# Kernel tuning notes

Hardware: AMD Instinct MI355X
Metric: run time of the kernel (lower is better)

The kernel has to match this reference:

```python
import jax, jax.numpy as jnp
import numpy as np

N_HEAD = 16
ROPE_BASE = 10000.0


def _rope(x, cos, sin):
    # x: [B,H,T,D]; cos/sin: [T,D/2] broadcast over B,H
    half = x.shape[-1] // 2
    x1, x2 = x[..., :half], x[..., half:]
    return jnp.concatenate([x1 * cos - x2 * sin, x1 * sin + x2 * cos], axis=-1)


def setup_inputs() -> dict:
    key = jax.random.key(0)
    k1, k2, k3 = jax.random.split(key, 3)
    C = 2048
    x = jax.random.normal(k1, (4, 2048, C), dtype=jnp.float32)
    w_qkv = jax.random.normal(k2, (C, 3 * C), dtype=jnp.float32) * 0.02
    w_proj = jax.random.normal(k3, (C, C), dtype=jnp.float32) * 0.02
    return {"x": x, "w_qkv": w_qkv, "w_proj": w_proj}


def reference(x, w_qkv, w_proj):
    B, T, C = x.shape
    H = N_HEAD
    D = C // H
    half = D // 2

    qkv = x @ w_qkv  # [B,T,3C]
    q, k, v = jnp.split(qkv, 3, axis=-1)
    # [B,T,C] -> [B,H,T,D]
    q = q.reshape(B, T, H, D).transpose(0, 2, 1, 3)
    k = k.reshape(B, T, H, D).transpose(0, 2, 1, 3)
    v = v.reshape(B, T, H, D).transpose(0, 2, 1, 3)

    # RoPE cache (start_pos = 0, no kv_cache / prefill path)
    inv_freq = 1.0 / (ROPE_BASE ** (jnp.arange(half, dtype=jnp.float32) / half))
    pos = jnp.arange(T, dtype=jnp.float32)
    freqs = pos[:, None] * inv_freq[None, :]  # [T, half]
    cos, sin = jnp.cos(freqs), jnp.sin(freqs)

    q = _rope(q, cos, sin)
    k = _rope(k, cos, sin)

    # scaled dot-product attention with explicit causal mask
    att = jnp.einsum("bhqd,bhkd->bhqk", q, k) / jnp.sqrt(jnp.asarray(D, x.dtype))
    causal = jnp.arange(T)[:, None] >= jnp.arange(T)[None, :]  # [T,T] bool
    att = jnp.where(causal, att, jnp.asarray(-jnp.inf, att.dtype))
    att = jax.nn.softmax(att, axis=-1)
    # dropout = identity (eval mode)
    out = jnp.einsum("bhqk,bhkd->bhqd", att, v)
    out = out.transpose(0, 2, 1, 3).reshape(B, T, C)
    out = out @ w_proj
    return out, k, v  # (output, new kv-cache)
```

## Files before the change

kernel.cpp:

```cpp
#include <hip/hip_runtime.h>
#include <math.h>

#define CDIM 2048
#define TDIM 2048
#define BDIM 4
#define HDIM 16
#define DDIM 128
#define M1   (BDIM * TDIM)
#define N1   (3 * CDIM)
#define KK   CDIM

typedef unsigned short u16;
typedef __bf16 bf16x8 __attribute__((ext_vector_type(8)));
typedef float f32x4 __attribute__((ext_vector_type(4)));

__device__ __forceinline__ u16 f2b(float f) {
  union { float f; unsigned u; } x; x.f = f;
  unsigned r = x.u + 0x7fffu + ((x.u >> 16) & 1u);
  return (u16)(r >> 16);
}

__device__ __forceinline__ void gload_lds16(const void* g, void* l) {
  __builtin_amdgcn_global_load_lds(
      (__attribute__((address_space(1))) void*)g,
      (__attribute__((address_space(3))) void*)l, 16, 0, 0);
}

__global__ void convert_x(const float* __restrict__ x, u16* __restrict__ xb, int n4) {
  int i = blockIdx.x * blockDim.x + threadIdx.x;
  if (i < n4) {
    float4 v = ((const float4*)x)[i];
    unsigned long long o = (unsigned long long)f2b(v.x)
                         | ((unsigned long long)f2b(v.y) << 16)
                         | ((unsigned long long)f2b(v.z) << 32)
                         | ((unsigned long long)f2b(v.w) << 48);
    ((unsigned long long*)xb)[i] = o;
  }
}

__global__ void transpose_w(const float* __restrict__ w, u16* __restrict__ wt, int K, int N) {
  __shared__ float tile[32][33];
  const int n0 = blockIdx.x * 32, k0 = blockIdx.y * 32;
  const int tx = threadIdx.x & 31, ty = threadIdx.x >> 5;
  for (int r = ty; r < 32; r += 8)
    tile[r][tx] = w[(k0 + r) * N + n0 + tx];
  __syncthreads();
  for (int r = ty; r < 32; r += 8)
    wt[(n0 + r) * K + k0 + tx] = f2b(tile[tx][r]);
}

__global__ void rope_tab(float* __restrict__ cosT, float* __restrict__ sinT) {
  int i = blockIdx.x * blockDim.x + threadIdx.x;
  int t = i >> 6, d = i & 63;
  double inv = pow(10000.0, -(double)d / 64.0);
  double a = (double)t * inv;
  cosT[i] = (float)cos(a);
  sinT[i] = (float)sin(a);
}

__global__ void transpose_v(const float* __restrict__ v, u16* __restrict__ vt) {
  __shared__ float tile[32][33];
  const int bh = blockIdx.z;
  const int t0 = blockIdx.x * 32, d0 = blockIdx.y * 32;
  const int tx = threadIdx.x & 31, ty = threadIdx.x >> 5;
  const float* src = v + (bh * TDIM + t0) * DDIM + d0;
  for (int r = ty; r < 32; r += 8)
    tile[r][tx] = src[r * DDIM + tx];
  __syncthreads();
  u16* dst = vt + (bh * DDIM + d0) * TDIM + t0;
  for (int r = ty; r < 32; r += 8)
    dst[r * TDIM + tx] = f2b(tile[tx][r]);
}

__global__ __launch_bounds__(256, 2) void gemm_qkv(
    const u16* __restrict__ A,
    const u16* __restrict__ Bt,
    const float* __restrict__ cosT, const float* __restrict__ sinT,
    u16* __restrict__ qb, u16* __restrict__ kb,
    float* __restrict__ kout, float* __restrict__ vout)
{
  __shared__ __attribute__((aligned(16))) union {
    struct { u16 A[128 * 32]; u16 B[128 * 32]; } st;
    float c[64 * 128];
  } sm;
  const int tid = threadIdx.x;
  const int wave = tid >> 6, lane = tid & 63;
  const int quad = lane >> 4, c16 = lane & 15;
  const int m0 = blockIdx.y * 128, n0 = blockIdx.x * 128;
  const int wm = (wave >> 1) * 64, wn = (wave & 1) * 64;

  f32x4 acc[4][4];
  f32x4 zero = {0.f, 0.f, 0.f, 0.f};
#pragma unroll
  for (int i = 0; i < 4; ++i)
#pragma unroll
    for (int j = 0; j < 4; ++j) acc[i][j] = zero;

  const u16* Ab = A + m0 * KK;
  const u16* Bb = Bt + n0 * KK;
  const int rowA = wave * 16 + (lane >> 2);
  const int kof = (lane & 3) * 8;

  for (int k0 = 0; k0 < KK; k0 += 32) {
#pragma unroll
    for (int r = 0; r < 2; ++r) {
      gload_lds16(Ab + (r * 64 + rowA) * KK + k0 + kof, &sm.st.A[(r * 64 + wave * 16) * 32]);
      gload_lds16(Bb + (r * 64 + rowA) * KK + k0 + kof, &sm.st.B[(r * 64 + wave * 16) * 32]);
    }
    __syncthreads();
    bf16x8 af[4], bf_[4];
#pragma unroll
    for (int i = 0; i < 4; ++i) af[i]  = *(const bf16x8*)&sm.st.A[(wm + i * 16 + c16) * 32 + quad * 8];
#pragma unroll
    for (int j = 0; j < 4; ++j) bf_[j] = *(const bf16x8*)&sm.st.B[(wn + j * 16 + c16) * 32 + quad * 8];
#pragma unroll
    for (int i = 0; i < 4; ++i)
#pragma unroll
      for (int j = 0; j < 4; ++j)
        acc[i][j] = __builtin_amdgcn_mfma_f32_16x16x32_bf16(af[i], bf_[j], acc[i][j], 0, 0, 0);
    __syncthreads();
  }

  const int mat = n0 >> 11;
  const int h = (n0 & 2047) >> 7;
  const float qscale = 0.088388347648318447f;
  for (int pass = 0; pass < 2; ++pass) {
    __syncthreads();
    if ((wave >> 1) == pass) {
#pragma unroll
      for (int i = 0; i < 4; ++i)
#pragma unroll
        for (int j = 0; j < 4; ++j)
#pragma unroll
          for (int r = 0; r < 4; ++r)
            sm.c[(i * 16 + quad * 4 + r) * 128 + wn + j * 16 + c16] = acc[i][j][r];
    }
    __syncthreads();
    for (int it = 0; it < 16; ++it) {
      int p = it * 256 + tid;
      int lr = p >> 6;
      int d = p & 63;
      float x1 = sm.c[lr * 128 + d];
      float x2 = sm.c[lr * 128 + 64 + d];
      int mg = m0 + pass * 64 + lr;
      int b = mg >> 11, t = mg & 2047;
      int idx = ((b * HDIM + h) * TDIM + t) * DDIM + d;
      if (mat == 2) {
        vout[idx] = x1; vout[idx + 64] = x2;
      } else {
        float cs = cosT[t * 64 + d], sn = sinT[t * 64 + d];
        float o1 = x1 * cs - x2 * sn;
        float o2 = x1 * sn + x2 * cs;
        if (mat == 0) {
          qb[idx] = f2b(o1 * qscale); qb[idx + 64] = f2b(o2 * qscale);
        } else {
          kout[idx] = o1; kout[idx + 64] = o2;
          kb[idx] = f2b(o1); kb[idx + 64] = f2b(o2);
        }
      }
    }
  }
}

__global__ __launch_bounds__(256, 2) void attn(
    const u16* __restrict__ qb, const u16* __restrict__ kb,
    const u16* __restrict__ vt, u16* __restrict__ att)
{
  __shared__ __attribute__((aligned(16))) u16 sh[24576];
  u16* const ksm = sh;
  u16* const vsm = sh + 8192;
  u16* const psm = sh + 16384;

  const int tid = threadIdx.x, wave = tid >> 6, lane = tid & 63;
  const int quad = lane >> 4, c16 = lane & 15;
  const int bx = blockIdx.x;
  const int bh = blockIdx.y;

  for (int hv = 0; hv < 2; ++hv) {
    const int qt = hv ? (7 - bx) : (bx + 8);
    const int q0 = qt * 128;

    {
      const u16* qg = qb + (bh * TDIM + q0) * DDIM;
      const int rowl = wave * 4 + (lane >> 4);
      const int ch = lane & 15;
#pragma unroll
      for (int r = 0; r < 8; ++r) {
        int row = r * 16 + rowl;
        gload_lds16(qg + row * DDIM + (ch ^ (row & 15)) * 8,
                    &sh[(r * 16 + wave * 4) * 128]);
      }
    }
    __syncthreads();
    bf16x8 qf[2][4];
#pragma unroll
    for (int g = 0; g < 2; ++g)
#pragma unroll
      for (int kp = 0; kp < 4; ++kp)
        qf[g][kp] = *(const bf16x8*)&sh[(g * 64 + wave * 16 + c16) * 128 +
                                        (((kp * 4 + quad) ^ c16) * 8)];
    __syncthreads();

    f32x4 o[2][8];
    f32x4 zero = {0.f, 0.f, 0.f, 0.f};
#pragma unroll
    for (int g = 0; g < 2; ++g)
#pragma unroll
      for (int jd = 0; jd < 8; ++jd) o[g][jd] = zero;
    float mrow[2][4], lrow[2][4];
#pragma unroll
    for (int g = 0; g < 2; ++g)
#pragma unroll
      for (int r = 0; r < 4; ++r) { mrow[g][r] = -INFINITY; lrow[g][r] = 0.f; }

    const int nchunk = 2 * qt + 2;
    for (int kc = 0; kc < nchunk; ++kc) {
      const int kc0 = kc * 64;
      {
        const u16* kg = kb + (bh * TDIM + kc0) * DDIM;
        const int rowl = wave * 4 + (lane >> 4);
        const int ch = lane & 15;
#pragma unroll
        for (int r = 0; r < 4; ++r) {
          int row = r * 16 + rowl;
          gload_lds16(kg + row * DDIM + (ch ^ (row & 15)) * 8,
                      &ksm[(r * 16 + wave * 4) * 128]);
        }
        const u16* vg = vt + bh * (DDIM * TDIM) + kc0;
        const int rowv = wave * 8 + (lane >> 3);
        const int chv = lane & 7;
#pragma unroll
        for (int r = 0; r < 4; ++r) {
          int row = r * 32 + rowv;
          gload_lds16(vg + row * TDIM + (chv ^ (row & 7)) * 8,
                      &vsm[(r * 32 + wave * 8) * 64]);
        }
      }
      __syncthreads();

      f32x4 st[2][4];
#pragma unroll
      for (int g = 0; g < 2; ++g)
#pragma unroll
        for (int j = 0; j < 4; ++j) st[g][j] = zero;
#pragma unroll
      for (int kp = 0; kp < 4; ++kp) {
#pragma unroll
        for (int j = 0; j < 4; ++j) {
          bf16x8 bk = *(const bf16x8*)&ksm[(j * 16 + c16) * 128 +
                                           (((kp * 4 + quad) ^ c16) * 8)];
          st[0][j] = __builtin_amdgcn_mfma_f32_16x16x32_bf16(qf[0][kp], bk, st[0][j], 0, 0, 0);
          st[1][j] = __builtin_amdgcn_mfma_f32_16x16x32_bf16(qf[1][kp], bk, st[1][j], 0, 0, 0);
        }
      }

      u16* const pw = psm + wave * 2048;
      float al2[2][4];
#pragma unroll
      for (int g = 0; g < 2; ++g) {
        const bool dg = (kc >= 2 * qt + g);
        const int qrow_base = q0 + g * 64 + wave * 16 + quad * 4;
#pragma unroll
        for (int r = 0; r < 4; ++r) {
          float mx = -INFINITY;
#pragma unroll
          for (int j = 0; j < 4; ++j) {
            float sv = st[g][j][r];
            if (dg && (kc0 + j * 16 + c16 > qrow_base + r)) sv = -INFINITY;
            st[g][j][r] = sv;
            mx = fmaxf(mx, sv);
          }
          mx = fmaxf(mx, __shfl_xor(mx, 1, 64));
          mx = fmaxf(mx, __shfl_xor(mx, 2, 64));
          mx = fmaxf(mx, __shfl_xor(mx, 4, 64));
          mx = fmaxf(mx, __shfl_xor(mx, 8, 64));
          float mnew = fmaxf(mrow[g][r], mx);
          float al = __expf(mrow[g][r] - mnew);
          mrow[g][r] = mnew;
          al2[g][r] = al;
          float sum = 0.f;
          const int row16 = quad * 4 + r;
#pragma unroll
          for (int j = 0; j < 4; ++j) {
            float p = __expf(st[g][j][r] - mnew);
            sum += p;
            int chunk = (j * 2 + (c16 >> 3)) ^ (row16 & 7);
            pw[g * 1024 + row16 * 64 + chunk * 8 + (c16 & 7)] = f2b(p);
          }
          sum += __shfl_xor(sum, 1, 64);
          sum += __shfl_xor(sum, 2, 64);
          sum += __shfl_xor(sum, 4, 64);
          sum += __shfl_xor(sum, 8, 64);
          lrow[g][r] = lrow[g][r] * al + sum;
        }
#pragma unroll
        for (int jd = 0; jd < 8; ++jd)
#pragma unroll
          for (int r = 0; r < 4; ++r)
            o[g][jd][r] *= al2[g][r];
      }

      asm volatile("s_waitcnt lgkmcnt(0)" ::: "memory");

#pragma unroll
      for (int s = 0; s < 2; ++s) {
        const int chp = ((s * 4 + quad) ^ (c16 & 7)) * 8;
        bf16x8 ap0 = *(const bf16x8*)&pw[c16 * 64 + chp];
        bf16x8 ap1 = *(const bf16x8*)&pw[1024 + c16 * 64 + chp];
#pragma unroll
        for (int jd = 0; jd < 8; ++jd) {
          bf16x8 bv = *(const bf16x8*)&vsm[(jd * 16 + c16) * 64 + chp];
          o[0][jd] = __builtin_amdgcn_mfma_f32_16x16x32_bf16(ap0, bv, o[0][jd], 0, 0, 0);
          o[1][jd] = __builtin_amdgcn_mfma_f32_16x16x32_bf16(ap1, bv, o[1][jd], 0, 0, 0);
        }
      }
      __syncthreads();
    }

    const int b = bh >> 4, h = bh & 15;
#pragma unroll
    for (int g = 0; g < 2; ++g) {
      float ri[4];
#pragma unroll
      for (int r = 0; r < 4; ++r) ri[r] = 1.f / lrow[g][r];
#pragma unroll
      for (int jd = 0; jd < 8; ++jd)
#pragma unroll
        for (int r = 0; r < 4; ++r) {
          int t = q0 + g * 64 + wave * 16 + quad * 4 + r;
          att[(b * TDIM + t) * CDIM + h * DDIM + jd * 16 + c16] = f2b(o[g][jd][r] * ri[r]);
        }
    }
  }
}

__global__ __launch_bounds__(256, 2) void gemm_proj(
    const u16* __restrict__ A,
    const u16* __restrict__ Bt,
    float* __restrict__ out)
{
  __shared__ __attribute__((aligned(16))) struct { u16 A[128 * 32]; u16 B[128 * 32]; } sm;
  const int tid = threadIdx.x;
  const int wave = tid >> 6, lane = tid & 63;
  const int quad = lane >> 4, c16 = lane & 15;
  const int m0 = blockIdx.y * 128, n0 = blockIdx.x * 128;
  const int wm = (wave >> 1) * 64, wn = (wave & 1) * 64;

  f32x4 acc[4][4];
  f32x4 zero = {0.f, 0.f, 0.f, 0.f};
#pragma unroll
  for (int i = 0; i < 4; ++i)
#pragma unroll
    for (int j = 0; j < 4; ++j) acc[i][j] = zero;

  const u16* Ab = A + m0 * KK;
  const u16* Bb = Bt + n0 * KK;
  const int rowA = wave * 16 + (lane >> 2);
  const int kof = (lane & 3) * 8;

  for (int k0 = 0; k0 < KK; k0 += 32) {
#pragma unroll
    for (int r = 0; r < 2; ++r) {
      gload_lds16(Ab + (r * 64 + rowA) * KK + k0 + kof, &sm.A[(r * 64 + wave * 16) * 32]);
      gload_lds16(Bb + (r * 64 + rowA) * KK + k0 + kof, &sm.B[(r * 64 + wave * 16) * 32]);
    }
    __syncthreads();
    bf16x8 af[4], bf_[4];
#pragma unroll
    for (int i = 0; i < 4; ++i) af[i]  = *(const bf16x8*)&sm.A[(wm + i * 16 + c16) * 32 + quad * 8];
#pragma unroll
    for (int j = 0; j < 4; ++j) bf_[j] = *(const bf16x8*)&sm.B[(wn + j * 16 + c16) * 32 + quad * 8];
#pragma unroll
    for (int i = 0; i < 4; ++i)
#pragma unroll
      for (int j = 0; j < 4; ++j)
        acc[i][j] = __builtin_amdgcn_mfma_f32_16x16x32_bf16(af[i], bf_[j], acc[i][j], 0, 0, 0);
    __syncthreads();
  }

#pragma unroll
  for (int i = 0; i < 4; ++i)
#pragma unroll
    for (int j = 0; j < 4; ++j)
#pragma unroll
      for (int r = 0; r < 4; ++r)
        out[(m0 + wm + i * 16 + quad * 4 + r) * CDIM + n0 + wn + j * 16 + c16] = acc[i][j][r];
}

extern "C" void kernel_launch(void* const* d_in, const int* in_sizes, int n_in,
                              void* d_out, int out_size, void* d_ws, size_t ws_size,
                              hipStream_t stream) {
  (void)in_sizes; (void)n_in; (void)out_size; (void)ws_size;
  const float* x      = (const float*)d_in[0];
  const float* w_qkv  = (const float*)d_in[1];
  const float* w_proj = (const float*)d_in[2];
  float* out  = (float*)d_out;
  float* kout = out + 16777216;
  float* vout = out + 2 * 16777216;

  char* ws = (char*)d_ws;
  u16*   xb     = (u16*)(ws);
  u16*   wqkvT  = (u16*)(ws + 33554432);
  u16*   wprojT = (u16*)(ws + 58720256);
  float* cosT   = (float*)(ws + 67108864);
  float* sinT   = (float*)(ws + 67633152);
  u16*   qb     = (u16*)(ws + 68157440);
  u16*   kb     = (u16*)(ws + 101711872);
  u16*   vt     = (u16*)(ws + 135266304);
  u16*   att    = xb;

  convert_x<<<16384, 256, 0, stream>>>(x, xb, 4194304);
  transpose_w<<<dim3(192, 64), 256, 0, stream>>>(w_qkv, wqkvT, KK, N1);
  transpose_w<<<dim3(64, 64), 256, 0, stream>>>(w_proj, wprojT, KK, CDIM);
  rope_tab<<<512, 256, 0, stream>>>(cosT, sinT);
  gemm_qkv<<<dim3(48, 64), 256, 0, stream>>>(xb, wqkvT, cosT, sinT, qb, kb, kout, vout);
  transpose_v<<<dim3(64, 4, 64), 256, 0, stream>>>(vout, vt);
  attn<<<dim3(8, 64), 256, 0, stream>>>(qb, kb, vt, att);
  gemm_proj<<<dim3(16, 64), 256, 0, stream>>>(att, wprojT, out);
}
```

Measured before the change: 810.1 us.

## Rewrite QKV and projection GEMMs with 256x256 tiles, double-buffered swizzled LDS

Replaces the 128x128, 256-thread GEMMs with 256x256 tiles on 512 threads and a K step of 64. LDS is double-buffered, so the next tile loads while MFMAs run, and it uses an XOR swizzle to avoid bank conflicts. The change also adds wave priority hints and a grouped block-order swizzle for L2 reuse. This cuts global traffic per FLOP and hides load latency, at the cost of 128KB of dynamic LDS, heavier register pressure, and fewer blocks (768 and 256), which may fill the CUs unevenly.

```diff
diff --git a/kernel.cpp b/kernel.cpp
--- a/kernel.cpp
+++ b/kernel.cpp
@@ -9,6 +9,7 @@
 #define M1   (BDIM * TDIM)
 #define N1   (3 * CDIM)
 #define KK   CDIM
+#define NT   32
 
 typedef unsigned short u16;
 typedef __bf16 bf16x8 __attribute__((ext_vector_type(8)));
@@ -72,78 +73,185 @@
     dst[r * TDIM + tx] = f2b(tile[tx][r]);
 }
 
-__global__ __launch_bounds__(256, 2) void gemm_qkv(
+
+#define GEMM256_MAINLOOP(APTR, BPTR)                                           \
+  const int rA = lane >> 3, cA = lane & 7;                                     \
+  const int stgrow = wave * 8 + rA;                                            \
+  const int stgoff = stgrow * KK + ((cA ^ rA) * 8);                            \
+  const u16* Ag = (APTR) + m0 * KK + stgoff;                                   \
+  const u16* Bg = (BPTR) + n0 * KK + stgoff;                                   \
+  const int ldsw = wave * 512;                                  \
+  f32x4 acc[8][4];                                                             \
+  {                                                                            \
+    f32x4 z = {0.f, 0.f, 0.f, 0.f};                                            \
+    _Pragma("unroll")                                                          \
+    for (int i = 0; i < 8; ++i)                                                \
+      _Pragma("unroll")                                                        \
+      for (int j = 0; j < 4; ++j) acc[i][j] = z;                               \
+  }                                                                            \
+                                         \
+  _Pragma("unroll")                                                            \
+  for (int i = 0; i < 4; ++i) {                                                \
+    gload_lds16(Ag + i * 64 * KK, &lds[i * 4096 + ldsw]);                      \
+    gload_lds16(Bg + i * 64 * KK, &lds[32768 + i * 4096 + ldsw]);              \
+  }                                                                            \
+  __syncthreads();                                                             \
+  const int rsw = c16 & 7;                               \
+  for (int kt = 0; kt < NT; ++kt) {                                            \
+    const int cur = kt & 1;                                                    \
+    const u16* bufA = &lds[cur * 16384];                                       \
+    const u16* bufB = &lds[32768 + cur * 16384];                               \
+    u16* nA = &lds[(cur ^ 1) * 16384];                                         \
+    u16* nB = &lds[32768 + (cur ^ 1) * 16384];                                 \
+    const u16* Agn = Ag + (kt + 1) * 64;                                       \
+    const u16* Bgn = Bg + (kt + 1) * 64;                                       \
+    const bool pre = (kt + 1 < NT);                                            \
+    bf16x8 afr[4][2], bfr[2][2], bfr2[2][2];                                   \
+                                          \
+    _Pragma("unroll")                                                          \
+    for (int i = 0; i < 4; ++i)                                                \
+      _Pragma("unroll")                                                        \
+      for (int kh = 0; kh < 2; ++kh)                                           \
+        afr[i][kh] = *(const bf16x8*)&bufA[(wm + i * 16 + c16) * 64 +          \
+                                           (((kh * 4 + quad) ^ rsw) * 8)];     \
+    _Pragma("unroll")                                                          \
+    for (int j = 0; j < 2; ++j)                                                \
+      _Pragma("unroll")                                                        \
+      for (int kh = 0; kh < 2; ++kh)                                           \
+        bfr[j][kh] = *(const bf16x8*)&bufB[(wn + j * 16 + c16) * 64 +          \
+                                           (((kh * 4 + quad) ^ rsw) * 8)];     \
+    if (pre) {                                                                 \
+      _Pragma("unroll")                                                        \
+      for (int i = 0; i < 4; ++i)                                              \
+        gload_lds16(Agn + i * 64 * KK, &nA[i * 4096 + ldsw]);                  \
+    }                                                                          \
+    __builtin_amdgcn_s_barrier();                                              \
+    asm volatile("s_waitcnt lgkmcnt(0)" ::: "memory");                         \
+    __builtin_amdgcn_s_setprio(1);                                             \
+    _Pragma("unroll")                                                          \
+    for (int i = 0; i < 4; ++i)                                                \
+      _Pragma("unroll")                                                        \
+      for (int j = 0; j < 2; ++j)                                              \
+        _Pragma("unroll")                                                      \
+        for (int kh = 0; kh < 2; ++kh)                                         \
+          acc[i][j] = __builtin_amdgcn_mfma_f32_16x16x32_bf16(                 \
+              afr[i][kh], bfr[j][kh], acc[i][j], 0, 0, 0);                     \
+    __builtin_amdgcn_s_setprio(0);                                             \
+    __builtin_amdgcn_s_barrier();                                              \
+                                          \
+    _Pragma("unroll")                                                          \
+    for (int j = 0; j < 2; ++j)                                                \
+      _Pragma("unroll")                                                        \
+      for (int kh = 0; kh < 2; ++kh)                                           \
+        bfr2[j][kh] = *(const bf16x8*)&bufB[(wn + (2 + j) * 16 + c16) * 64 +   \
+                                            (((kh * 4 + quad) ^ rsw) * 8)];    \
+    if (pre) {                                                                 \
+      _Pragma("unroll")                                                        \
+      for (int i = 0; i < 4; ++i)                                              \
+        gload_lds16(Bgn + i * 64 * KK, &nB[i * 4096 + ldsw]);                  \
+    }                                                                          \
+    __builtin_amdgcn_s_barrier();                                              \
+    asm volatile("s_waitcnt lgkmcnt(0)" ::: "memory");                         \
+    __builtin_amdgcn_s_setprio(1);                                             \
+    _Pragma("unroll")                                                          \
+    for (int i = 0; i < 4; ++i)                                                \
+      _Pragma("unroll")                                                        \
+      for (int j = 0; j < 2; ++j)                                              \
+        _Pragma("unroll")                                                      \
+        for (int kh = 0; kh < 2; ++kh)                                         \
+          acc[i][2 + j] = __builtin_amdgcn_mfma_f32_16x16x32_bf16(             \
+              afr[i][kh], bfr2[j][kh], acc[i][2 + j], 0, 0, 0);                \
+    __builtin_amdgcn_s_setprio(0);                                             \
+    __builtin_amdgcn_s_barrier();                                              \
+                                          \
+    _Pragma("unroll")                                                          \
+    for (int i = 0; i < 4; ++i)                                                \
+      _Pragma("unroll")                                                        \
+      for (int kh = 0; kh < 2; ++kh)                                           \
+        afr[i][kh] = *(const bf16x8*)&bufA[(wm + (4 + i) * 16 + c16) * 64 +    \
+                                           (((kh * 4 + quad) ^ rsw) * 8)];     \
+    __builtin_amdgcn_s_barrier();                                              \
+    asm volatile("s_waitcnt lgkmcnt(0)" ::: "memory");                         \
+    __builtin_amdgcn_s_setprio(1);                                             \
+    _Pragma("unroll")                                                          \
+    for (int i = 0; i < 4; ++i)                                                \
+      _Pragma("unroll")                                                        \
+      for (int j = 0; j < 2; ++j)                                              \
+        _Pragma("unroll")                                                      \
+        for (int kh = 0; kh < 2; ++kh)                                         \
+          acc[4 + i][2 + j] = __builtin_amdgcn_mfma_f32_16x16x32_bf16(         \
+              afr[i][kh], bfr2[j][kh], acc[4 + i][2 + j], 0, 0, 0);            \
+    __builtin_amdgcn_s_setprio(0);                                             \
+    __builtin_amdgcn_s_barrier();                                              \
+                                          \
+    _Pragma("unroll")                                                          \
+    for (int j = 0; j < 2; ++j)                                                \
+      _Pragma("unroll")                                                        \
+      for (int kh = 0; kh < 2; ++kh)                                           \
+        bfr[j][kh] = *(const bf16x8*)&bufB[(wn + j * 16 + c16) * 64 +          \
+                                           (((kh * 4 + quad) ^ rsw) * 8)];     \
+    __builtin_amdgcn_s_barrier();                                              \
+    asm volatile("s_waitcnt lgkmcnt(0)" ::: "memory");                         \
+    __builtin_amdgcn_s_setprio(1);                                             \
+    _Pragma("unroll")                                                          \
+    for (int i = 0; i < 4; ++i)                                                \
+      _Pragma("unroll")                                                        \
+      for (int j = 0; j < 2; ++j)                                              \
+        _Pragma("unroll")                                                      \
+        for (int kh = 0; kh < 2; ++kh)                                         \
+          acc[4 + i][j] = __builtin_amdgcn_mfma_f32_16x16x32_bf16(             \
+              afr[i][kh], bfr[j][kh], acc[4 + i][j], 0, 0, 0);                 \
+    __builtin_amdgcn_s_setprio(0);                                             \
+        \
+    __syncthreads();                                                           \
+  }
+
+__global__ __launch_bounds__(512, 2) void gemm_qkv(
     const u16* __restrict__ A,
     const u16* __restrict__ Bt,
     const float* __restrict__ cosT, const float* __restrict__ sinT,
     u16* __restrict__ qb, u16* __restrict__ kb,
     float* __restrict__ kout, float* __restrict__ vout)
 {
-  __shared__ __attribute__((aligned(16))) union {
-    struct { u16 A[128 * 32]; u16 B[128 * 32]; } st;
-    float c[64 * 128];
-  } sm;
-  const int tid = threadIdx.x;
-  const int wave = tid >> 6, lane = tid & 63;
+  extern __shared__ __align__(16) u16 lds[];
+  const int tid = threadIdx.x, wave = tid >> 6, lane = tid & 63;
   const int quad = lane >> 4, c16 = lane & 15;
-  const int m0 = blockIdx.y * 128, n0 = blockIdx.x * 128;
-  const int wm = (wave >> 1) * 64, wn = (wave & 1) * 64;
-
-  f32x4 acc[4][4];
-  f32x4 zero = {0.f, 0.f, 0.f, 0.f};
-#pragma unroll
-  for (int i = 0; i < 4; ++i)
-#pragma unroll
-    for (int j = 0; j < 4; ++j) acc[i][j] = zero;
-
-  const u16* Ab = A + m0 * KK;
-  const u16* Bb = Bt + n0 * KK;
-  const int rowA = wave * 16 + (lane >> 2);
-  const int kof = (lane & 3) * 8;
-
-  for (int k0 = 0; k0 < KK; k0 += 32) {
-#pragma unroll
-    for (int r = 0; r < 2; ++r) {
-      gload_lds16(Ab + (r * 64 + rowA) * KK + k0 + kof, &sm.st.A[(r * 64 + wave * 16) * 32]);
-      gload_lds16(Bb + (r * 64 + rowA) * KK + k0 + kof, &sm.st.B[(r * 64 + wave * 16) * 32]);
+  const int bid = blockIdx.y * 24 + blockIdx.x;
+  const int swz = (bid & 7) * 96 + (bid >> 3);
+  const int m0 = (swz / 24) * 256, n0 = (swz % 24) * 256;
+  const int wm = (wave >> 2) * 128, wn = (wave & 3) * 64;
+
+  GEMM256_MAINLOOP(A, Bt)
+
+  float* cbuf = (float*)lds;
+  const int mat = n0 >> 11;
+  const int hbase = (n0 & 2047) >> 7;
+  const float qscale = 0.088388347648318447f;
+  for (int pass = 0; pass < 4; ++pass) {
+    __syncthreads();
+    if ((wave >> 2) == (pass >> 1)) {
+#pragma unroll
+      for (int i = 0; i < 4; ++i) {
+        const int mf = (pass & 1) * 4 + i;
+#pragma unroll
+        for (int j = 0; j < 4; ++j)
+#pragma unroll
+          for (int r = 0; r < 4; ++r)
+            cbuf[(i * 16 + quad * 4 + r) * 260 + wn + j * 16 + c16] = acc[mf][j][r];
+      }
     }
     __syncthreads();
-    bf16x8 af[4], bf_[4];
-#pragma unroll
-    for (int i = 0; i < 4; ++i) af[i]  = *(const bf16x8*)&sm.st.A[(wm + i * 16 + c16) * 32 + quad * 8];
-#pragma unroll
-    for (int j = 0; j < 4; ++j) bf_[j] = *(const bf16x8*)&sm.st.B[(wn + j * 16 + c16) * 32 + quad * 8];
-#pragma unroll
-    for (int i = 0; i < 4; ++i)
-#pragma unroll
-      for (int j = 0; j < 4; ++j)
-        acc[i][j] = __builtin_amdgcn_mfma_f32_16x16x32_bf16(af[i], bf_[j], acc[i][j], 0, 0, 0);
-    __syncthreads();
-  }
-
-  const int mat = n0 >> 11;
-  const int h = (n0 & 2047) >> 7;
-  const float qscale = 0.088388347648318447f;
-  for (int pass = 0; pass < 2; ++pass) {
-    __syncthreads();
-    if ((wave >> 1) == pass) {
-#pragma unroll
-      for (int i = 0; i < 4; ++i)
-#pragma unroll
-        for (int j = 0; j < 4; ++j)
-#pragma unroll
-          for (int r = 0; r < 4; ++r)
-            sm.c[(i * 16 + quad * 4 + r) * 128 + wn + j * 16 + c16] = acc[i][j][r];
-    }
-    __syncthreads();
+#pragma unroll
     for (int it = 0; it < 16; ++it) {
-      int p = it * 256 + tid;
-      int lr = p >> 6;
+      int p = it * 512 + tid;
+      int lr = p >> 7;
+      int hc = (p >> 6) & 1;
       int d = p & 63;
-      float x1 = sm.c[lr * 128 + d];
-      float x2 = sm.c[lr * 128 + 64 + d];
+      float x1 = cbuf[lr * 260 + hc * 128 + d];
+      float x2 = cbuf[lr * 260 + hc * 128 + 64 + d];
       int mg = m0 + pass * 64 + lr;
       int b = mg >> 11, t = mg & 2047;
+      int h = hbase + hc;
       int idx = ((b * HDIM + h) * TDIM + t) * DDIM + d;
       if (mat == 2) {
         vout[idx] = x1; vout[idx + 64] = x2;
@@ -160,6 +268,31 @@
       }
     }
   }
+}
+
+__global__ __launch_bounds__(512, 2) void gemm_proj(
+    const u16* __restrict__ A,
+    const u16* __restrict__ Bt,
+    float* __restrict__ out)
+{
+  extern __shared__ __align__(16) u16 lds[];
+  const int tid = threadIdx.x, wave = tid >> 6, lane = tid & 63;
+  const int quad = lane >> 4, c16 = lane & 15;
+  const int bid = blockIdx.y * 8 + blockIdx.x;
+  const int swz = (bid & 7) * 32 + (bid >> 3);
+  const int m0 = (swz >> 3) * 256, n0 = (swz & 7) * 256;
+  const int wm = (wave >> 2) * 128, wn = (wave & 3) * 64;
+
+  GEMM256_MAINLOOP(A, Bt)
+
+#pragma unroll
+  for (int mf = 0; mf < 8; ++mf)
+#pragma unroll
+    for (int nf = 0; nf < 4; ++nf)
+#pragma unroll
+      for (int r = 0; r < 4; ++r)
+        out[(m0 + wm + mf * 16 + quad * 4 + r) * CDIM + n0 + wn + nf * 16 + c16] =
+            acc[mf][nf][r];
 }
 
 __global__ __launch_bounds__(256, 2) void attn(
@@ -334,59 +467,6 @@
   }
 }
 
-__global__ __launch_bounds__(256, 2) void gemm_proj(
-    const u16* __restrict__ A,
-    const u16* __restrict__ Bt,
-    float* __restrict__ out)
-{
-  __shared__ __attribute__((aligned(16))) struct { u16 A[128 * 32]; u16 B[128 * 32]; } sm;
-  const int tid = threadIdx.x;
-  const int wave = tid >> 6, lane = tid & 63;
-  const int quad = lane >> 4, c16 = lane & 15;
-  const int m0 = blockIdx.y * 128, n0 = blockIdx.x * 128;
-  const int wm = (wave >> 1) * 64, wn = (wave & 1) * 64;
-
-  f32x4 acc[4][4];
-  f32x4 zero = {0.f, 0.f, 0.f, 0.f};
-#pragma unroll
-  for (int i = 0; i < 4; ++i)
-#pragma unroll
-    for (int j = 0; j < 4; ++j) acc[i][j] = zero;
-
-  const u16* Ab = A + m0 * KK;
-  const u16* Bb = Bt + n0 * KK;
-  const int rowA = wave * 16 + (lane >> 2);
-  const int kof = (lane & 3) * 8;
-
-  for (int k0 = 0; k0 < KK; k0 += 32) {
-#pragma unroll
-    for (int r = 0; r < 2; ++r) {
-      gload_lds16(Ab + (r * 64 + rowA) * KK + k0 + kof, &sm.A[(r * 64 + wave * 16) * 32]);
-      gload_lds16(Bb + (r * 64 + rowA) * KK + k0 + kof, &sm.B[(r * 64 + wave * 16) * 32]);
-    }
-    __syncthreads();
-    bf16x8 af[4], bf_[4];
-#pragma unroll
-    for (int i = 0; i < 4; ++i) af[i]  = *(const bf16x8*)&sm.A[(wm + i * 16 + c16) * 32 + quad * 8];
-#pragma unroll
-    for (int j = 0; j < 4; ++j) bf_[j] = *(const bf16x8*)&sm.B[(wn + j * 16 + c16) * 32 + quad * 8];
-#pragma unroll
-    for (int i = 0; i < 4; ++i)
-#pragma unroll
-      for (int j = 0; j < 4; ++j)
-        acc[i][j] = __builtin_amdgcn_mfma_f32_16x16x32_bf16(af[i], bf_[j], acc[i][j], 0, 0, 0);
-    __syncthreads();
-  }
-
-#pragma unroll
-  for (int i = 0; i < 4; ++i)
-#pragma unroll
-    for (int j = 0; j < 4; ++j)
-#pragma unroll
-      for (int r = 0; r < 4; ++r)
-        out[(m0 + wm + i * 16 + quad * 4 + r) * CDIM + n0 + wn + j * 16 + c16] = acc[i][j][r];
-}
-
 extern "C" void kernel_launch(void* const* d_in, const int* in_sizes, int n_in,
                               void* d_out, int out_size, void* d_ws, size_t ws_size,
                               hipStream_t stream) {
@@ -409,12 +489,21 @@
   u16*   vt     = (u16*)(ws + 135266304);
   u16*   att    = xb;
 
+  static int attr_set = 0;
+  if (!attr_set) {
+    hipFuncSetAttribute((const void*)gemm_qkv,
+                        hipFuncAttributeMaxDynamicSharedMemorySize, 131072);
+    hipFuncSetAttribute((const void*)gemm_proj,
+                        hipFuncAttributeMaxDynamicSharedMemorySize, 131072);
+    attr_set = 1;
+  }
+
   convert_x<<<16384, 256, 0, stream>>>(x, xb, 4194304);
   transpose_w<<<dim3(192, 64), 256, 0, stream>>>(w_qkv, wqkvT, KK, N1);
   transpose_w<<<dim3(64, 64), 256, 0, stream>>>(w_proj, wprojT, KK, CDIM);
   rope_tab<<<512, 256, 0, stream>>>(cosT, sinT);
-  gemm_qkv<<<dim3(48, 64), 256, 0, stream>>>(xb, wqkvT, cosT, sinT, qb, kb, kout, vout);
+  gemm_qkv<<<dim3(24, 32), 512, 131072, stream>>>(xb, wqkvT, cosT, sinT, qb, kb, kout, vout);
   transpose_v<<<dim3(64, 4, 64), 256, 0, stream>>>(vout, vt);
   attn<<<dim3(8, 64), 256, 0, stream>>>(qb, kb, vt, att);
-  gemm_proj<<<dim3(16, 64), 256, 0, stream>>>(att, wprojT, out);
-}
+  gemm_proj<<<dim3(8, 32), 512, 131072, stream>>>(att, wprojT, out);
+}
```

Measured after the change: 1.670 ms. 106% more time.
